# Performance work log

Hardware: AMD Instinct MI355X
Metric: run time of the kernel (lower is better)

## Reference

```python
import jax, jax.numpy as jnp
import numpy as np

EMB = 768
HEADS = 12
HEAD_DIM = EMB // HEADS
LN_EPS = 1e-5


def _layernorm(x, g, b):
    mu = jnp.mean(x, axis=-1, keepdims=True)
    var = jnp.mean(jnp.square(x - mu), axis=-1, keepdims=True)
    return (x - mu) * jax.lax.rsqrt(var + LN_EPS) * g + b


def _att_block(x, ln_g, ln_b, w_qkv, b_qkv, w_proj, b_proj):
    # x: [b, n, e]
    B, N, E = x.shape
    h, d = HEADS, HEAD_DIM
    qkv = _layernorm(x, ln_g, ln_b) @ w_qkv.T + b_qkv          # [b, n, 3e]
    # einops 'b n (h d qkv)': last axis factors as (h, d, 3), qkv innermost
    qkv = qkv.reshape(B, N, h, d, 3)
    qkv = jnp.moveaxis(qkv, (4, 2), (0, 2))                    # [3, b, h, n, d]
    q, k, v = qkv[0], qkv[1], qkv[2]
    scale = d ** (-0.5)
    # NOTE: original code DIVIDES by scale (= multiplies by sqrt(d)) -- faithful
    scores = jnp.einsum('bhqd,bhkd->bhqk', q, k) / scale       # [b, h, n, n]
    attn = jax.nn.softmax(scores, axis=-1)
    out = jnp.einsum('bhqk,bhkd->bhqd', attn, v)               # [b, h, n, d]
    out = out.transpose(0, 2, 1, 3).reshape(B, N, E)           # [b, n, e]
    return x + out @ w_proj.T + b_proj


def setup_inputs() -> dict:
    key = jax.random.key(0)
    ks = jax.random.split(key, 8)
    B, N, E = 2, 2048, EMB
    s = E ** (-0.5)
    return {
        'modal1': jax.random.normal(ks[0], (B, N, E), jnp.float32),
        'modal2': jax.random.normal(ks[1], (B, N, E), jnp.float32),
        'ln1_g': jnp.ones((E,), jnp.float32),
        'ln1_b': jnp.zeros((E,), jnp.float32),
        'w_qkv1': jax.random.normal(ks[2], (3 * E, E), jnp.float32) * s,
        'b_qkv1': jnp.zeros((3 * E,), jnp.float32),
        'w_proj1': jax.random.normal(ks[3], (E, E), jnp.float32) * s,
        'b_proj1': jnp.zeros((E,), jnp.float32),
        'ln2_g': jnp.ones((E,), jnp.float32),
        'ln2_b': jnp.zeros((E,), jnp.float32),
        'w_qkv2': jax.random.normal(ks[4], (3 * E, E), jnp.float32) * s,
        'b_qkv2': jnp.zeros((3 * E,), jnp.float32),
        'w_proj2': jax.random.normal(ks[5], (E, E), jnp.float32) * s,
        'b_proj2': jnp.zeros((E,), jnp.float32),
    }


def reference(modal1, modal2, ln1_g, ln1_b, w_qkv1, b_qkv1, w_proj1, b_proj1,
              ln2_g, ln2_b, w_qkv2, b_qkv2, w_proj2, b_proj2):
    out1 = _att_block(modal1, ln1_g, ln1_b, w_qkv1, b_qkv1, w_proj1, b_proj1)
    out2 = _att_block(modal2, ln2_g, ln2_b, w_qkv2, b_qkv2, w_proj2, b_proj2)
    return (out1, out2)
```

## Files before the change

kernel.cpp:

```cpp
#include <hip/hip_runtime.h>
#include <hip/hip_bf16.h>


typedef unsigned short u16;
typedef unsigned int   u32;
typedef __attribute__((ext_vector_type(4))) float          floatx4;
typedef __attribute__((ext_vector_type(8))) short          shortx8;

#define EMB   768
#define SEQ   2048
#define NHEAD 12
#define HDIM  64
#define RPM   4096
#define NROW  8192
#define NUNIT 48
#define LDA   40
#define LDK   72

__device__ __forceinline__ float bf2f(u16 h) {
  union { u32 u; float f; } v; v.u = ((u32)h) << 16; return v.f;
}
__device__ __forceinline__ u16 f2bf(float f) {
  union { float f; u32 u; } v; v.f = f;
  u32 r = v.u + 0x7fffu + ((v.u >> 16) & 1u);
  return (u16)(r >> 16);
}
__device__ __forceinline__ u16 f2bf_tr(float f) {
  union { float f; u32 u; } v; v.f = f;
  return (u16)(v.u >> 16);
}
__device__ __forceinline__ float swz_max16(float v) {
  union { float f; int i; } a;
  a.f = v; a.i = __builtin_amdgcn_ds_swizzle(a.i, 0x041F); v = fmaxf(v, a.f);
  a.f = v; a.i = __builtin_amdgcn_ds_swizzle(a.i, 0x081F); v = fmaxf(v, a.f);
  a.f = v; a.i = __builtin_amdgcn_ds_swizzle(a.i, 0x101F); v = fmaxf(v, a.f);
  a.f = v; a.i = __builtin_amdgcn_ds_swizzle(a.i, 0x201F); v = fmaxf(v, a.f);
  return v;
}

__global__ __launch_bounds__(256) void prep_wq(
    const float* __restrict__ wq1, const float* __restrict__ wq2,
    u16* __restrict__ wh, u16* __restrict__ wl)
{
  int bx = blockIdx.x;
  int modal = bx / 2304, rowp = bx % 2304;
  int typ = rowp / 768, hd = rowp % 768;
  const float* W = (modal ? wq2 : wq1) + (size_t)(hd * 3 + typ) * EMB;
  size_t dst = (size_t)bx * EMB;
  int t = threadIdx.x;
  #pragma unroll
  for (int i = 0; i < 3; ++i) {
    int e = t + i * 256;
    float v = W[e];
    u16 h = f2bf(v);
    wh[dst + e] = h;
    wl[dst + e] = f2bf(v - bf2f(h));
  }
}

__global__ __launch_bounds__(256) void prep_wp(
    const float* __restrict__ wp1, const float* __restrict__ wp2,
    u16* __restrict__ wh)
{
  int bx = blockIdx.x;
  int modal = bx / 768, row = bx % 768;
  const float* W = (modal ? wp2 : wp1) + (size_t)row * EMB;
  size_t dst = (size_t)bx * EMB;
  int t = threadIdx.x;
  #pragma unroll
  for (int i = 0; i < 3; ++i) {
    int e = t + i * 256;
    wh[dst + e] = f2bf(W[e]);
  }
}

__global__ __launch_bounds__(256) void k_ln(
    const float* __restrict__ x1, const float* __restrict__ x2,
    const float* __restrict__ g1, const float* __restrict__ b1,
    const float* __restrict__ g2, const float* __restrict__ b2,
    u16* __restrict__ xn_hi, u16* __restrict__ xn_lo)
{
  int row = blockIdx.x;
  int modal = row >> 12;
  const float* x = modal ? x2 : x1;
  const float* g = modal ? g2 : g1;
  const float* bb = modal ? b2 : b1;
  int r = row & (RPM - 1);
  const float* xr = x + (size_t)r * EMB;
  int t = threadIdx.x;
  float v0 = xr[t], v1 = xr[t + 256], v2 = xr[t + 512];
  float s = v0 + v1 + v2;
  float s2 = v0 * v0 + v1 * v1 + v2 * v2;
  #pragma unroll
  for (int m = 1; m < 64; m <<= 1) { s += __shfl_xor(s, m); s2 += __shfl_xor(s2, m); }
  __shared__ float ls[4], ls2[4];
  int w = t >> 6;
  if ((t & 63) == 0) { ls[w] = s; ls2[w] = s2; }
  __syncthreads();
  s = ls[0] + ls[1] + ls[2] + ls[3];
  s2 = ls2[0] + ls2[1] + ls2[2] + ls2[3];
  float mu = s * (1.0f / EMB);
  float var = s2 * (1.0f / EMB) - mu * mu;
  float rs = rsqrtf(var + 1e-5f);
  size_t base = (size_t)row * EMB;
  float vv[3] = { v0, v1, v2 };
  #pragma unroll
  for (int i = 0; i < 3; ++i) {
    int e = t + i * 256;
    float xn = (vv[i] - mu) * rs * g[e] + bb[e];
    u16 h = f2bf(xn);
    xn_hi[base + e] = h;
    xn_lo[base + e] = f2bf(xn - bf2f(h));
  }
}

__global__ __launch_bounds__(256) void k_qkv(
    const u16* __restrict__ xn_hi, const u16* __restrict__ xn_lo,
    const u16* __restrict__ wqh, const u16* __restrict__ wql,
    const float* __restrict__ bq1, const float* __restrict__ bq2,
    u16* __restrict__ q_hi, u16* __restrict__ q_lo,
    u16* __restrict__ k_hi, u16* __restrict__ k_lo,
    u16* __restrict__ vT)
{
  int mt = blockIdx.x, ntile = blockIdx.y, modal = blockIdx.z;
  const float* BQ = modal ? bq2 : bq1;
  int typ = ntile / 6;
  int hd0 = (ntile % 6) * 128;

  __shared__ u16 As_hi[128 * LDA], As_lo[128 * LDA], Wh[128 * LDA], Wl[128 * LDA];

  int tid = threadIdx.x, lane = tid & 63, w = tid >> 6;
  int wm = (w >> 1) * 64, wn = (w & 1) * 64;
  int lc = lane & 15, lq = lane >> 4;

  floatx4 acc[4][4] = {};
  size_t arow0 = (size_t)(modal * RPM + mt * 128) * EMB;
  size_t wrow0 = (size_t)(modal * 2304 + typ * 768 + hd0) * EMB;

  for (int k0 = 0; k0 < EMB; k0 += 32) {
    #pragma unroll
    for (int i = 0; i < 2; ++i) {
      int c = tid + i * 256;
      int rr = c >> 2, cc = (c & 3) * 8;
      size_t go = (size_t)rr * EMB + k0 + cc;
      *(shortx8*)&As_hi[rr * LDA + cc] = *(const shortx8*)(xn_hi + arow0 + go);
      *(shortx8*)&Wh[rr * LDA + cc]    = *(const shortx8*)(wqh + wrow0 + go);
      if (typ != 2) {
        *(shortx8*)&As_lo[rr * LDA + cc] = *(const shortx8*)(xn_lo + arow0 + go);
        *(shortx8*)&Wl[rr * LDA + cc]    = *(const shortx8*)(wql + wrow0 + go);
      }
    }
    __syncthreads();
    shortx8 ah[4], al[4], wh[4], wl[4];
    #pragma unroll
    for (int i = 0; i < 4; ++i) {
      ah[i] = *(const shortx8*)&As_hi[(wm + i * 16 + lc) * LDA + lq * 8];
      wh[i] = *(const shortx8*)&Wh[(wn + i * 16 + lc) * LDA + lq * 8];
      if (typ != 2) {
        al[i] = *(const shortx8*)&As_lo[(wm + i * 16 + lc) * LDA + lq * 8];
        wl[i] = *(const shortx8*)&Wl[(wn + i * 16 + lc) * LDA + lq * 8];
      }
    }
    #pragma unroll
    for (int i = 0; i < 4; ++i)
      #pragma unroll
      for (int jn = 0; jn < 4; ++jn) {
        acc[i][jn] = __builtin_amdgcn_mfma_f32_16x16x32_bf16(ah[i], wh[jn], acc[i][jn], 0, 0, 0);
        if (typ != 2) {
          acc[i][jn] = __builtin_amdgcn_mfma_f32_16x16x32_bf16(al[i], wh[jn], acc[i][jn], 0, 0, 0);
          acc[i][jn] = __builtin_amdgcn_mfma_f32_16x16x32_bf16(ah[i], wl[jn], acc[i][jn], 0, 0, 0);
        }
      }
    __syncthreads();
  }

  #pragma unroll
  for (int i = 0; i < 4; ++i) {
    int mrow0 = mt * 128 + wm + i * 16 + lq * 4;
    #pragma unroll
    for (int jn = 0; jn < 4; ++jn) {
      int colp = hd0 + wn + jn * 16 + lc;
      int h = colp >> 6, d = colp & 63;
      float bias = BQ[colp * 3 + typ];
      #pragma unroll
      for (int r = 0; r < 4; ++r) {
        int mrow = mrow0 + r;
        int b = mrow >> 11, nq = mrow & (SEQ - 1);
        int uu = modal * 24 + b * 12 + h;
        float val = acc[i][jn][r] + bias;
        if (typ == 0) {
          size_t o = ((size_t)uu * SEQ + nq) * HDIM + d;
          u16 hh = f2bf(val); q_hi[o] = hh; q_lo[o] = f2bf(val - bf2f(hh));
        } else if (typ == 1) {
          size_t o = ((size_t)uu * SEQ + nq) * HDIM + d;
          u16 hh = f2bf(val); k_hi[o] = hh; k_lo[o] = f2bf(val - bf2f(hh));
        } else {
          vT[((size_t)uu * HDIM + d) * SEQ + nq] = f2bf(val);
        }
      }
    }
  }
}

__global__ __launch_bounds__(256) void k_attn(
    const u16* __restrict__ q_hi, const u16* __restrict__ q_lo,
    const u16* __restrict__ k_hi, const u16* __restrict__ k_lo,
    const u16* __restrict__ vT, u16* __restrict__ attn_out)
{
  int qt = blockIdx.x, u = blockIdx.y;
  __shared__ u16 Kh[64 * LDK], Kl[64 * LDK], Vs[64 * LDK];
  __shared__ u16 Ps[4][32 * LDK];

  int tid = threadIdx.x, lane = tid & 63, w = tid >> 6;
  int lc = lane & 15, lq = lane >> 4;
  u16* psw = &Ps[w][0];

  shortx8 qh[2][2], ql[2][2];
  #pragma unroll
  for (int mi = 0; mi < 2; ++mi) {
    size_t qb = ((size_t)u * SEQ + qt * 128 + w * 32 + mi * 16 + lc) * HDIM + lq * 8;
    qh[mi][0] = *(const shortx8*)(q_hi + qb);
    qh[mi][1] = *(const shortx8*)(q_hi + qb + 32);
    ql[mi][0] = *(const shortx8*)(q_lo + qb);
    ql[mi][1] = *(const shortx8*)(q_lo + qb + 32);
  }

  shortx8 ONES;
  #pragma unroll
  for (int j = 0; j < 8; ++j) ONES[j] = (short)0x3F80;

  floatx4 O[2][4] = {};
  floatx4 Osum[2] = {};
  float mrow[2][4];
  #pragma unroll
  for (int mi = 0; mi < 2; ++mi)
    #pragma unroll
    for (int r = 0; r < 4; ++r) mrow[mi][r] = -1e30f;
  const float Cs = 11.5415603271f;

  int c0 = tid, c1 = tid + 256;
  int r0 = c0 >> 3, cc0 = (c0 & 7) * 8;
  int r1 = c1 >> 3, cc1 = (c1 & 7) * 8;
  const u16* khp0 = k_hi + ((size_t)u * SEQ + r0) * HDIM + cc0;
  const u16* khp1 = k_hi + ((size_t)u * SEQ + r1) * HDIM + cc1;
  const u16* klp0 = k_lo + ((size_t)u * SEQ + r0) * HDIM + cc0;
  const u16* klp1 = k_lo + ((size_t)u * SEQ + r1) * HDIM + cc1;
  const u16* vp0  = vT + ((size_t)u * HDIM + r0) * SEQ + cc0;
  const u16* vp1  = vT + ((size_t)u * HDIM + r1) * SEQ + cc1;

  for (int kc = 0; kc < SEQ; kc += 64) {
    *(shortx8*)&Kh[r0 * LDK + cc0] = *(const shortx8*)(khp0 + (size_t)kc * HDIM);
    *(shortx8*)&Kh[r1 * LDK + cc1] = *(const shortx8*)(khp1 + (size_t)kc * HDIM);
    *(shortx8*)&Kl[r0 * LDK + cc0] = *(const shortx8*)(klp0 + (size_t)kc * HDIM);
    *(shortx8*)&Kl[r1 * LDK + cc1] = *(const shortx8*)(klp1 + (size_t)kc * HDIM);
    *(shortx8*)&Vs[r0 * LDK + cc0] = *(const shortx8*)(vp0 + kc);
    *(shortx8*)&Vs[r1 * LDK + cc1] = *(const shortx8*)(vp1 + kc);
    __syncthreads();

    floatx4 S[2][4] = {};
    #pragma unroll
    for (int nt = 0; nt < 4; ++nt)
      #pragma unroll
      for (int ks = 0; ks < 2; ++ks) {
        shortx8 kf = *(const shortx8*)&Kh[(nt * 16 + lc) * LDK + ks * 32 + lq * 8];
        shortx8 lf = *(const shortx8*)&Kl[(nt * 16 + lc) * LDK + ks * 32 + lq * 8];
        #pragma unroll
        for (int mi = 0; mi < 2; ++mi) {
          S[mi][nt] = __builtin_amdgcn_mfma_f32_16x16x32_bf16(qh[mi][ks], kf, S[mi][nt], 0, 0, 0);
          S[mi][nt] = __builtin_amdgcn_mfma_f32_16x16x32_bf16(ql[mi][ks], kf, S[mi][nt], 0, 0, 0);
          S[mi][nt] = __builtin_amdgcn_mfma_f32_16x16x32_bf16(qh[mi][ks], lf, S[mi][nt], 0, 0, 0);
        }
      }
    #pragma unroll
    for (int mi = 0; mi < 2; ++mi)
      #pragma unroll
      for (int nt = 0; nt < 4; ++nt) S[mi][nt] *= Cs;

    #pragma unroll
    for (int mi = 0; mi < 2; ++mi) {
      float alpha[4];
      #pragma unroll
      for (int r = 0; r < 4; ++r) {
        float mc = fmaxf(fmaxf(S[mi][0][r], S[mi][1][r]), fmaxf(S[mi][2][r], S[mi][3][r]));
        mc = swz_max16(mc);
        float mn = fmaxf(mrow[mi][r], mc);
        alpha[r] = __builtin_amdgcn_exp2f(mrow[mi][r] - mn);
        mrow[mi][r] = mn;
      }
      #pragma unroll
      for (int nt = 0; nt < 4; ++nt)
        #pragma unroll
        for (int r = 0; r < 4; ++r) {
          float e = __builtin_amdgcn_exp2f(S[mi][nt][r] - mrow[mi][r]);
          psw[(mi * 16 + lq * 4 + r) * LDK + nt * 16 + lc] = f2bf_tr(e);
        }
      #pragma unroll
      for (int nt = 0; nt < 4; ++nt)
        #pragma unroll
        for (int r = 0; r < 4; ++r) O[mi][nt][r] *= alpha[r];
      #pragma unroll
      for (int r = 0; r < 4; ++r) Osum[mi][r] *= alpha[r];
    }

    #pragma unroll
    for (int ks = 0; ks < 2; ++ks) {
      shortx8 pf[2];
      #pragma unroll
      for (int mi = 0; mi < 2; ++mi)
        pf[mi] = *(const shortx8*)&psw[(mi * 16 + lc) * LDK + ks * 32 + lq * 8];
      #pragma unroll
      for (int nt = 0; nt < 4; ++nt) {
        shortx8 vf = *(const shortx8*)&Vs[(nt * 16 + lc) * LDK + ks * 32 + lq * 8];
        #pragma unroll
        for (int mi = 0; mi < 2; ++mi)
          O[mi][nt] = __builtin_amdgcn_mfma_f32_16x16x32_bf16(pf[mi], vf, O[mi][nt], 0, 0, 0);
      }
      #pragma unroll
      for (int mi = 0; mi < 2; ++mi)
        Osum[mi] = __builtin_amdgcn_mfma_f32_16x16x32_bf16(pf[mi], ONES, Osum[mi], 0, 0, 0);
    }
    __syncthreads();
  }

  int modal = u / 24, b = (u / 12) & 1, h = u % 12;
  #pragma unroll
  for (int mi = 0; mi < 2; ++mi)
    #pragma unroll
    for (int r = 0; r < 4; ++r) {
      float rl = __builtin_amdgcn_rcpf(Osum[mi][r]);
      int qrow = qt * 128 + w * 32 + mi * 16 + lq * 4 + r;
      size_t ob = ((size_t)(modal * RPM + b * SEQ + qrow)) * EMB + h * 64 + lc;
      #pragma unroll
      for (int nt = 0; nt < 4; ++nt)
        attn_out[ob + nt * 16] = f2bf(O[mi][nt][r] * rl);
    }
}

__global__ __launch_bounds__(256) void k_proj(
    const u16* __restrict__ ao, const u16* __restrict__ wph,
    const float* __restrict__ x1, const float* __restrict__ x2,
    const float* __restrict__ bp1, const float* __restrict__ bp2,
    float* __restrict__ out)
{
  int mt = blockIdx.x, ntile = blockIdx.y, modal = blockIdx.z;
  const float* BP = modal ? bp2 : bp1;
  const float* x  = modal ? x2 : x1;

  __shared__ u16 As[128 * LDA], Ws[128 * LDA];
  int tid = threadIdx.x, lane = tid & 63, w = tid >> 6;
  int wm = (w >> 1) * 64, wn = (w & 1) * 64;
  int lc = lane & 15, lq = lane >> 4;

  floatx4 acc[4][4] = {};
  size_t arow0 = (size_t)(modal * RPM + mt * 128) * EMB;
  int col0 = ntile * 128;
  size_t wrow0 = (size_t)(modal * 768 + col0) * EMB;

  for (int k0 = 0; k0 < EMB; k0 += 32) {
    #pragma unroll
    for (int i = 0; i < 2; ++i) {
      int c = tid + i * 256;
      int rr = c >> 2, cc = (c & 3) * 8;
      size_t go = (size_t)rr * EMB + k0 + cc;
      *(shortx8*)&As[rr * LDA + cc] = *(const shortx8*)(ao + arow0 + go);
      *(shortx8*)&Ws[rr * LDA + cc] = *(const shortx8*)(wph + wrow0 + go);
    }
    __syncthreads();
    shortx8 af[4], wf[4];
    #pragma unroll
    for (int i = 0; i < 4; ++i) {
      af[i] = *(const shortx8*)&As[(wm + i * 16 + lc) * LDA + lq * 8];
      wf[i] = *(const shortx8*)&Ws[(wn + i * 16 + lc) * LDA + lq * 8];
    }
    #pragma unroll
    for (int i = 0; i < 4; ++i)
      #pragma unroll
      for (int jn = 0; jn < 4; ++jn)
        acc[i][jn] = __builtin_amdgcn_mfma_f32_16x16x32_bf16(af[i], wf[jn], acc[i][jn], 0, 0, 0);
    __syncthreads();
  }

  #pragma unroll
  for (int i = 0; i < 4; ++i) {
    int mrow0 = mt * 128 + wm + i * 16 + lq * 4;
    #pragma unroll
    for (int jn = 0; jn < 4; ++jn) {
      int col = col0 + wn + jn * 16 + lc;
      float bias = BP[col];
      #pragma unroll
      for (int r = 0; r < 4; ++r) {
        int mrow = mrow0 + r;
        float val = acc[i][jn][r] + bias + x[(size_t)mrow * EMB + col];
        out[((size_t)(modal * RPM + mrow)) * EMB + col] = val;
      }
    }
  }
}

extern "C" void kernel_launch(void* const* d_in, const int* in_sizes, int n_in,
                              void* d_out, int out_size, void* d_ws, size_t ws_size,
                              hipStream_t stream) {
  const float* modal1 = (const float*)d_in[0];
  const float* modal2 = (const float*)d_in[1];
  const float* ln1_g  = (const float*)d_in[2];
  const float* ln1_b  = (const float*)d_in[3];
  const float* w_qkv1 = (const float*)d_in[4];
  const float* b_qkv1 = (const float*)d_in[5];
  const float* w_proj1= (const float*)d_in[6];
  const float* b_proj1= (const float*)d_in[7];
  const float* ln2_g  = (const float*)d_in[8];
  const float* ln2_b  = (const float*)d_in[9];
  const float* w_qkv2 = (const float*)d_in[10];
  const float* b_qkv2 = (const float*)d_in[11];
  const float* w_proj2= (const float*)d_in[12];
  const float* b_proj2= (const float*)d_in[13];
  float* out = (float*)d_out;

  const size_t BUFE = (size_t)NROW * EMB;
  const size_t WQE  = (size_t)2 * 2304 * EMB;
  u16* xn_hi = (u16*)d_ws;
  u16* xn_lo = xn_hi + BUFE;
  u16* q_hi  = xn_lo + BUFE;
  u16* q_lo  = q_hi + BUFE;
  u16* k_hi  = q_lo + BUFE;
  u16* k_lo  = k_hi + BUFE;
  u16* vT    = k_lo + BUFE;
  u16* wq_h  = vT + BUFE;
  u16* wq_l  = wq_h + WQE;
  u16* attn  = xn_hi;
  u16* wp_h  = q_lo;

  prep_wq<<<4608, 256, 0, stream>>>(w_qkv1, w_qkv2, wq_h, wq_l);
  k_ln<<<NROW, 256, 0, stream>>>(modal1, modal2, ln1_g, ln1_b, ln2_g, ln2_b, xn_hi, xn_lo);
  dim3 g2(32, 18, 2);
  k_qkv<<<g2, 256, 0, stream>>>(xn_hi, xn_lo, wq_h, wq_l, b_qkv1, b_qkv2,
                                q_hi, q_lo, k_hi, k_lo, vT);
  dim3 g3(16, 48);
  k_attn<<<g3, 256, 0, stream>>>(q_hi, q_lo, k_hi, k_lo, vT, attn);
  prep_wp<<<1536, 256, 0, stream>>>(w_proj1, w_proj2, wp_h);
  dim3 g4(32, 6, 2);
  k_proj<<<g4, 256, 0, stream>>>(attn, wp_h, modal1, modal2, b_proj1, b_proj2, out);
}
```

Measured before the change: 411.4 us.

## Rewrite attention kernel with 32x32 MFMA, async LDS double buffering, lazy rescale

Restructures the flash-attention kernel to use 32x32x16 bf16 MFMAs, computing S transposed so the P fragments stay in registers via packed bf16 conversion and a permlane32 swap instead of an LDS round trip. K_hi, K_lo and V tiles are staged with global_load_lds into swizzled, double-buffered shared memory so the next tile loads while the current one computes. The row sum is kept in registers instead of an extra MFMA against a ones vector. The running max is only rescaled when it grows past a threshold, and occupancy is requested via launch bounds. The threshold trick lets exponent values exceed 1 before rescaling, and the larger register footprint is a risk.

```diff
diff --git a/kernel.cpp b/kernel.cpp
--- a/kernel.cpp
+++ b/kernel.cpp
@@ -4,8 +4,10 @@
 
 typedef unsigned short u16;
 typedef unsigned int   u32;
-typedef __attribute__((ext_vector_type(4))) float          floatx4;
-typedef __attribute__((ext_vector_type(8))) short          shortx8;
+typedef __attribute__((ext_vector_type(4)))  float floatx4;
+typedef __attribute__((ext_vector_type(16))) float floatx16;
+typedef __attribute__((ext_vector_type(8)))  short shortx8;
+typedef __attribute__((ext_vector_type(2)))  unsigned int uintx2;
 
 #define EMB   768
 #define SEQ   2048
@@ -15,7 +17,7 @@
 #define NROW  8192
 #define NUNIT 48
 #define LDA   40
-#define LDK   72
+#define KTS   4096
 
 __device__ __forceinline__ float bf2f(u16 h) {
   union { u32 u; float f; } v; v.u = ((u32)h) << 16; return v.f;
@@ -25,17 +27,22 @@
   u32 r = v.u + 0x7fffu + ((v.u >> 16) & 1u);
   return (u16)(r >> 16);
 }
-__device__ __forceinline__ u16 f2bf_tr(float f) {
-  union { float f; u32 u; } v; v.f = f;
-  return (u16)(v.u >> 16);
-}
-__device__ __forceinline__ float swz_max16(float v) {
-  union { float f; int i; } a;
-  a.f = v; a.i = __builtin_amdgcn_ds_swizzle(a.i, 0x041F); v = fmaxf(v, a.f);
-  a.f = v; a.i = __builtin_amdgcn_ds_swizzle(a.i, 0x081F); v = fmaxf(v, a.f);
-  a.f = v; a.i = __builtin_amdgcn_ds_swizzle(a.i, 0x101F); v = fmaxf(v, a.f);
-  a.f = v; a.i = __builtin_amdgcn_ds_swizzle(a.i, 0x201F); v = fmaxf(v, a.f);
-  return v;
+__device__ __forceinline__ u32 cvtpk_bf16(float a, float b) {
+  u32 r;
+  asm("v_cvt_pk_bf16_f32 %0, %1, %2" : "=v"(r) : "v"(a), "v"(b));
+  return r;
+}
+__device__ __forceinline__ void swap_halves(u32 a, u32 b, u32& x, u32& y) {
+#if __has_builtin(__builtin_amdgcn_permlane32_swap)
+  uintx2 r = __builtin_amdgcn_permlane32_swap(a, b, false, false);
+  x = r.x; y = r.y;
+#else
+  u32 ax = (u32)__shfl_xor((int)a, 32);
+  u32 bx = (u32)__shfl_xor((int)b, 32);
+  bool h = (threadIdx.x & 32) != 0;
+  x = h ? bx : a;
+  y = h ? b : ax;
+#endif
 }
 
 __global__ __launch_bounds__(256) void prep_wq(
@@ -202,138 +209,167 @@
   }
 }
 
-__global__ __launch_bounds__(256) void k_attn(
+__global__ __launch_bounds__(256, 3) void k_attn(
     const u16* __restrict__ q_hi, const u16* __restrict__ q_lo,
     const u16* __restrict__ k_hi, const u16* __restrict__ k_lo,
     const u16* __restrict__ vT, u16* __restrict__ attn_out)
 {
   int qt = blockIdx.x, u = blockIdx.y;
-  __shared__ u16 Kh[64 * LDK], Kl[64 * LDK], Vs[64 * LDK];
-  __shared__ u16 Ps[4][32 * LDK];
+  __shared__ u16 lds[2][3 * KTS];
 
   int tid = threadIdx.x, lane = tid & 63, w = tid >> 6;
-  int lc = lane & 15, lq = lane >> 4;
-  u16* psw = &Ps[w][0];
-
-  shortx8 qh[2][2], ql[2][2];
-  #pragma unroll
-  for (int mi = 0; mi < 2; ++mi) {
-    size_t qb = ((size_t)u * SEQ + qt * 128 + w * 32 + mi * 16 + lc) * HDIM + lq * 8;
-    qh[mi][0] = *(const shortx8*)(q_hi + qb);
-    qh[mi][1] = *(const shortx8*)(q_hi + qb + 32);
-    ql[mi][0] = *(const shortx8*)(q_lo + qb);
-    ql[mi][1] = *(const shortx8*)(q_lo + qb + 32);
-  }
-
-  shortx8 ONES;
-  #pragma unroll
-  for (int j = 0; j < 8; ++j) ONES[j] = (short)0x3F80;
-
-  floatx4 O[2][4] = {};
-  floatx4 Osum[2] = {};
-  float mrow[2][4];
-  #pragma unroll
-  for (int mi = 0; mi < 2; ++mi)
-    #pragma unroll
-    for (int r = 0; r < 4; ++r) mrow[mi][r] = -1e30f;
+  int col = lane & 31, hi = lane >> 5;
+  int swz = (col & 7) << 4;
+
+  shortx8 qh[4], qlo[4];
+  {
+    size_t qb = ((size_t)u * SEQ + qt * 128 + w * 32 + col) * HDIM + hi * 8;
+    #pragma unroll
+    for (int s = 0; s < 4; ++s) {
+      qh[s]  = *(const shortx8*)(q_hi + qb + s * 16);
+      qlo[s] = *(const shortx8*)(q_lo + qb + s * 16);
+    }
+  }
+
+  int lrow = lane >> 3;
+  int lcol = ((lane & 7) ^ lrow) << 3;
+  const u16* kh_src = k_hi + (size_t)u * SEQ * HDIM;
+  const u16* kl_src = k_lo + (size_t)u * SEQ * HDIM;
+  const u16* v_src  = vT  + (size_t)u * HDIM * SEQ;
+
+  auto stage = [&](int buf, int kc) {
+    #pragma unroll
+    for (int c = 0; c < 6; ++c) {
+      int seg = w * 6 + c;
+      int tile = seg >> 3, segin = seg & 7;
+      u16* dst = &lds[buf][tile * KTS + segin * 512];
+      const u16* src;
+      if (tile == 0)      src = kh_src + (size_t)(kc + segin * 8 + lrow) * HDIM + lcol;
+      else if (tile == 1) src = kl_src + (size_t)(kc + segin * 8 + lrow) * HDIM + lcol;
+      else                src = v_src  + (size_t)(segin * 8 + lrow) * SEQ + kc + lcol;
+      __builtin_amdgcn_global_load_lds(
+          (const __attribute__((address_space(1))) unsigned int*)src,
+          (__attribute__((address_space(3))) unsigned int*)dst, 16, 0, 0);
+    }
+  };
+
+  floatx16 O0 = {}, O1 = {};
+  float m_r = -1e30f, lsum = 0.0f;
   const float Cs = 11.5415603271f;
-
-  int c0 = tid, c1 = tid + 256;
-  int r0 = c0 >> 3, cc0 = (c0 & 7) * 8;
-  int r1 = c1 >> 3, cc1 = (c1 & 7) * 8;
-  const u16* khp0 = k_hi + ((size_t)u * SEQ + r0) * HDIM + cc0;
-  const u16* khp1 = k_hi + ((size_t)u * SEQ + r1) * HDIM + cc1;
-  const u16* klp0 = k_lo + ((size_t)u * SEQ + r0) * HDIM + cc0;
-  const u16* klp1 = k_lo + ((size_t)u * SEQ + r1) * HDIM + cc1;
-  const u16* vp0  = vT + ((size_t)u * HDIM + r0) * SEQ + cc0;
-  const u16* vp1  = vT + ((size_t)u * HDIM + r1) * SEQ + cc1;
-
-  for (int kc = 0; kc < SEQ; kc += 64) {
-    *(shortx8*)&Kh[r0 * LDK + cc0] = *(const shortx8*)(khp0 + (size_t)kc * HDIM);
-    *(shortx8*)&Kh[r1 * LDK + cc1] = *(const shortx8*)(khp1 + (size_t)kc * HDIM);
-    *(shortx8*)&Kl[r0 * LDK + cc0] = *(const shortx8*)(klp0 + (size_t)kc * HDIM);
-    *(shortx8*)&Kl[r1 * LDK + cc1] = *(const shortx8*)(klp1 + (size_t)kc * HDIM);
-    *(shortx8*)&Vs[r0 * LDK + cc0] = *(const shortx8*)(vp0 + kc);
-    *(shortx8*)&Vs[r1 * LDK + cc1] = *(const shortx8*)(vp1 + kc);
+  const float THR = 8.0f;
+
+  stage(0, 0);
+  __syncthreads();
+
+  for (int t = 0; t < SEQ / 64; ++t) {
+    int cur = t & 1;
+    if (t + 1 < SEQ / 64) stage(cur ^ 1, (t + 1) * 64);
+
+    const char* Kh = (const char*)&lds[cur][0];
+    const char* Kl = (const char*)&lds[cur][KTS];
+    const char* Vt = (const char*)&lds[cur][2 * KTS];
+
+    floatx16 S0 = {}, S1 = {};
+    __builtin_amdgcn_s_setprio(1);
+    #pragma unroll
+    for (int s = 0; s < 4; ++s) {
+      int cb = (s * 32 + hi * 16) ^ swz;
+      shortx8 kf0 = *(const shortx8*)(Kh + col * 128 + cb);
+      shortx8 kl0 = *(const shortx8*)(Kl + col * 128 + cb);
+      shortx8 kf1 = *(const shortx8*)(Kh + (32 + col) * 128 + cb);
+      shortx8 kl1 = *(const shortx8*)(Kl + (32 + col) * 128 + cb);
+      S0 = __builtin_amdgcn_mfma_f32_32x32x16_bf16(kf0, qh[s],  S0, 0, 0, 0);
+      S1 = __builtin_amdgcn_mfma_f32_32x32x16_bf16(kf1, qh[s],  S1, 0, 0, 0);
+      S0 = __builtin_amdgcn_mfma_f32_32x32x16_bf16(kf0, qlo[s], S0, 0, 0, 0);
+      S1 = __builtin_amdgcn_mfma_f32_32x32x16_bf16(kf1, qlo[s], S1, 0, 0, 0);
+      S0 = __builtin_amdgcn_mfma_f32_32x32x16_bf16(kl0, qh[s],  S0, 0, 0, 0);
+      S1 = __builtin_amdgcn_mfma_f32_32x32x16_bf16(kl1, qh[s],  S1, 0, 0, 0);
+    }
+    __builtin_amdgcn_s_setprio(0);
+
+    float tm[16];
+    #pragma unroll
+    for (int r = 0; r < 16; ++r) tm[r] = fmaxf(S0[r], S1[r]);
+    #pragma unroll
+    for (int st = 8; st >= 1; st >>= 1)
+      #pragma unroll
+      for (int i = 0; i < st; ++i) tm[i] = fmaxf(tm[i], tm[i + st]);
+    float mx = tm[0] * Cs;
+    mx = fmaxf(mx, __shfl_xor(mx, 32));
+
+    if (!__all(mx <= m_r + THR)) {
+      float mn = fmaxf(m_r, mx);
+      float alpha = __builtin_amdgcn_exp2f(m_r - mn);
+      m_r = mn;
+      lsum *= alpha;
+      #pragma unroll
+      for (int r = 0; r < 16; ++r) {
+        int qsrc = (r & 3) + 8 * (r >> 2) + 4 * hi;
+        union { float f; int i; } a; a.f = alpha;
+        a.i = __builtin_amdgcn_ds_bpermute(qsrc << 2, a.i);
+        O0[r] *= a.f; O1[r] *= a.f;
+      }
+    }
+
+    #pragma unroll
+    for (int r = 0; r < 16; ++r) {
+      S0[r] = __builtin_amdgcn_exp2f(fmaf(Cs, S0[r], -m_r));
+      S1[r] = __builtin_amdgcn_exp2f(fmaf(Cs, S1[r], -m_r));
+    }
+    #pragma unroll
+    for (int r = 0; r < 16; ++r) tm[r] = S0[r] + S1[r];
+    #pragma unroll
+    for (int st = 8; st >= 1; st >>= 1)
+      #pragma unroll
+      for (int i = 0; i < st; ++i) tm[i] += tm[i + st];
+    lsum += tm[0];
+
+    shortx8 pf[4];
+    #pragma unroll
+    for (int kt = 0; kt < 2; ++kt)
+      #pragma unroll
+      for (int h2 = 0; h2 < 2; ++h2) {
+        floatx16 Sv = kt ? S1 : S0;
+        int b0 = h2 * 8;
+        u32 A = cvtpk_bf16(Sv[b0 + 0], Sv[b0 + 1]);
+        u32 B = cvtpk_bf16(Sv[b0 + 2], Sv[b0 + 3]);
+        u32 C = cvtpk_bf16(Sv[b0 + 4], Sv[b0 + 5]);
+        u32 D = cvtpk_bf16(Sv[b0 + 6], Sv[b0 + 7]);
+        u32 w0, w1, w2, w3;
+        swap_halves(A, C, w0, w2);
+        swap_halves(B, D, w1, w3);
+        union { u32 uu[4]; shortx8 ss; } pk_;
+        pk_.uu[0] = w0; pk_.uu[1] = w1; pk_.uu[2] = w2; pk_.uu[3] = w3;
+        pf[kt * 2 + h2] = pk_.ss;
+      }
+
+    __builtin_amdgcn_s_setprio(1);
+    #pragma unroll
+    for (int ks = 0; ks < 4; ++ks) {
+      int cb = (ks * 32 + hi * 16) ^ swz;
+      shortx8 v0 = *(const shortx8*)(Vt + col * 128 + cb);
+      shortx8 v1 = *(const shortx8*)(Vt + (32 + col) * 128 + cb);
+      O0 = __builtin_amdgcn_mfma_f32_32x32x16_bf16(pf[ks], v0, O0, 0, 0, 0);
+      O1 = __builtin_amdgcn_mfma_f32_32x32x16_bf16(pf[ks], v1, O1, 0, 0, 0);
+    }
+    __builtin_amdgcn_s_setprio(0);
+
     __syncthreads();
-
-    floatx4 S[2][4] = {};
-    #pragma unroll
-    for (int nt = 0; nt < 4; ++nt)
-      #pragma unroll
-      for (int ks = 0; ks < 2; ++ks) {
-        shortx8 kf = *(const shortx8*)&Kh[(nt * 16 + lc) * LDK + ks * 32 + lq * 8];
-        shortx8 lf = *(const shortx8*)&Kl[(nt * 16 + lc) * LDK + ks * 32 + lq * 8];
-        #pragma unroll
-        for (int mi = 0; mi < 2; ++mi) {
-          S[mi][nt] = __builtin_amdgcn_mfma_f32_16x16x32_bf16(qh[mi][ks], kf, S[mi][nt], 0, 0, 0);
-          S[mi][nt] = __builtin_amdgcn_mfma_f32_16x16x32_bf16(ql[mi][ks], kf, S[mi][nt], 0, 0, 0);
-          S[mi][nt] = __builtin_amdgcn_mfma_f32_16x16x32_bf16(qh[mi][ks], lf, S[mi][nt], 0, 0, 0);
-        }
-      }
-    #pragma unroll
-    for (int mi = 0; mi < 2; ++mi)
-      #pragma unroll
-      for (int nt = 0; nt < 4; ++nt) S[mi][nt] *= Cs;
-
-    #pragma unroll
-    for (int mi = 0; mi < 2; ++mi) {
-      float alpha[4];
-      #pragma unroll
-      for (int r = 0; r < 4; ++r) {
-        float mc = fmaxf(fmaxf(S[mi][0][r], S[mi][1][r]), fmaxf(S[mi][2][r], S[mi][3][r]));
-        mc = swz_max16(mc);
-        float mn = fmaxf(mrow[mi][r], mc);
-        alpha[r] = __builtin_amdgcn_exp2f(mrow[mi][r] - mn);
-        mrow[mi][r] = mn;
-      }
-      #pragma unroll
-      for (int nt = 0; nt < 4; ++nt)
-        #pragma unroll
-        for (int r = 0; r < 4; ++r) {
-          float e = __builtin_amdgcn_exp2f(S[mi][nt][r] - mrow[mi][r]);
-          psw[(mi * 16 + lq * 4 + r) * LDK + nt * 16 + lc] = f2bf_tr(e);
-        }
-      #pragma unroll
-      for (int nt = 0; nt < 4; ++nt)
-        #pragma unroll
-        for (int r = 0; r < 4; ++r) O[mi][nt][r] *= alpha[r];
-      #pragma unroll
-      for (int r = 0; r < 4; ++r) Osum[mi][r] *= alpha[r];
-    }
-
-    #pragma unroll
-    for (int ks = 0; ks < 2; ++ks) {
-      shortx8 pf[2];
-      #pragma unroll
-      for (int mi = 0; mi < 2; ++mi)
-        pf[mi] = *(const shortx8*)&psw[(mi * 16 + lc) * LDK + ks * 32 + lq * 8];
-      #pragma unroll
-      for (int nt = 0; nt < 4; ++nt) {
-        shortx8 vf = *(const shortx8*)&Vs[(nt * 16 + lc) * LDK + ks * 32 + lq * 8];
-        #pragma unroll
-        for (int mi = 0; mi < 2; ++mi)
-          O[mi][nt] = __builtin_amdgcn_mfma_f32_16x16x32_bf16(pf[mi], vf, O[mi][nt], 0, 0, 0);
-      }
-      #pragma unroll
-      for (int mi = 0; mi < 2; ++mi)
-        Osum[mi] = __builtin_amdgcn_mfma_f32_16x16x32_bf16(pf[mi], ONES, Osum[mi], 0, 0, 0);
-    }
-    __syncthreads();
-  }
-
+  }
+
+  float lt = lsum + __shfl_xor(lsum, 32);
+  float rl = __builtin_amdgcn_rcpf(lt);
   int modal = u / 24, b = (u / 12) & 1, h = u % 12;
-  #pragma unroll
-  for (int mi = 0; mi < 2; ++mi)
-    #pragma unroll
-    for (int r = 0; r < 4; ++r) {
-      float rl = __builtin_amdgcn_rcpf(Osum[mi][r]);
-      int qrow = qt * 128 + w * 32 + mi * 16 + lq * 4 + r;
-      size_t ob = ((size_t)(modal * RPM + b * SEQ + qrow)) * EMB + h * 64 + lc;
-      #pragma unroll
-      for (int nt = 0; nt < 4; ++nt)
-        attn_out[ob + nt * 16] = f2bf(O[mi][nt][r] * rl);
-    }
+  size_t obase = ((size_t)(modal * RPM + b * SEQ + qt * 128 + w * 32)) * EMB + h * 64 + col;
+  #pragma unroll
+  for (int r = 0; r < 16; ++r) {
+    int ql_ = (r & 3) + 8 * (r >> 2) + 4 * hi;
+    union { float f; int i; } a; a.f = rl;
+    a.i = __builtin_amdgcn_ds_bpermute(ql_ << 2, a.i);
+    size_t ob = obase + (size_t)ql_ * EMB;
+    attn_out[ob]      = f2bf(O0[r] * a.f);
+    attn_out[ob + 32] = f2bf(O1[r] * a.f);
+  }
 }
 
 __global__ __launch_bounds__(256) void k_proj(
```

New measurement: 357.2 us. 1.15x faster.
